# Kernel optimization log

Hardware: AMD Instinct MI355X
Metric: run time of the kernel (lower is better)

## Reference

```python
import jax, jax.numpy as jnp
import numpy as np
import math

H = 16
D_MODEL = 1024
B, S = 2, 2048

def setup_inputs() -> dict:
    key = jax.random.key(0)
    ks = jax.random.split(key, 7)
    q = jax.random.normal(ks[0], (B, S, D_MODEL), dtype=jnp.float32)
    k = jax.random.normal(ks[1], (B, S, D_MODEL), dtype=jnp.float32)
    v = jax.random.normal(ks[2], (B, S, D_MODEL), dtype=jnp.float32)
    mask = jnp.ones((1, 1, S, S), dtype=jnp.int32)
    sc = 1.0 / math.sqrt(D_MODEL)
    W_Q = jax.random.normal(ks[3], (D_MODEL, D_MODEL), dtype=jnp.float32) * sc
    W_K = jax.random.normal(ks[4], (D_MODEL, D_MODEL), dtype=jnp.float32) * sc
    W_V = jax.random.normal(ks[5], (D_MODEL, D_MODEL), dtype=jnp.float32) * sc
    W_T = jax.random.normal(ks[6], (D_MODEL, D_MODEL), dtype=jnp.float32) * sc
    return {"q": q, "k": k, "v": v, "mask": mask, "W_Q": W_Q, "W_K": W_K, "W_V": W_V, "W_T": W_T}

def reference(q, k, v, mask, W_Q, W_K, W_V, W_T):
    # W matrices stored as (in, out); nn.Linear applies x @ W.T with W (out,in),
    # equivalent here since we treat these directly as projection matrices.
    def split_heads(x):  # [B,S,D] -> [B,H,S,hd]
        Bq, Sq, Dq = x.shape
        return x.reshape(Bq, Sq, H, Dq // H).transpose(0, 2, 1, 3)

    Q = split_heads(q @ W_Q)
    K = split_heads(k @ W_K)
    V = split_heads(v @ W_V)
    d_k = Q.shape[-1]
    score = jnp.einsum("bhqd,bhkd->bhqk", Q, K) / math.sqrt(d_k)
    score = jnp.where(mask == 0, jnp.float32(-1e9), score)
    attn = jax.nn.softmax(score, axis=-1)
    out = jnp.einsum("bhqk,bhkd->bhqd", attn, V)
    out = out.transpose(0, 2, 1, 3).reshape(q.shape[0], q.shape[1], D_MODEL)
    return out @ W_T
```

## Files before the change

kernel.cpp:

```cpp
#include <hip/hip_runtime.h>
#include <hip/hip_bf16.h>
#include <stdint.h>

#define H  16
#define DM 1024
#define BB 2
#define SS 2048
#define HD 64

#define QSCALE 0.18033688011112042f
#define MASKVAL -57.7078f

typedef __attribute__((ext_vector_type(8))) short bf16x8;
typedef __attribute__((ext_vector_type(4))) float f32x4;

__device__ __forceinline__ short f2bf(float f) {
  __hip_bfloat16 h = __float2bfloat16(f);
  return *reinterpret_cast<short*>(&h);
}

__device__ __forceinline__ unsigned pack_bf16(float a, float b) {
#if __has_builtin(__builtin_amdgcn_cvt_pk_bf16_f32)
  typedef __attribute__((ext_vector_type(2))) __bf16 bf16x2_t;
  bf16x2_t p = __builtin_amdgcn_cvt_pk_bf16_f32(a, b);
  unsigned u;
  __builtin_memcpy(&u, &p, 4);
  return u;
#else
  unsigned ua = __builtin_bit_cast(unsigned, a);
  unsigned ub = __builtin_bit_cast(unsigned, b);
  ua = (ua + 0x7FFFu + ((ua >> 16) & 1u)) >> 16;
  ub = (ub + 0x7FFFu + ((ub >> 16) & 1u));
  return (ub & 0xFFFF0000u) | ua;
#endif
}

__device__ __forceinline__ void load16_lds(const short* g, short* l) {
  __builtin_amdgcn_global_load_lds(
      (const __attribute__((address_space(1))) void*)g,
      (__attribute__((address_space(3))) void*)l, 16, 0, 0);
}

__global__ void prep_kernel(const float* __restrict__ Wq, const float* __restrict__ Wk,
                            const float* __restrict__ Wv, const float* __restrict__ Wt,
                            short* __restrict__ WTall,
                            const float* __restrict__ q, const float* __restrict__ k,
                            const float* __restrict__ v, short* __restrict__ Abf,
                            const int4* __restrict__ mask4, int* __restrict__ flag) {
  int z = blockIdx.z;
  int t = threadIdx.x;
  if (z < 4) {
    if (blockIdx.x >= 1024) return;
    __shared__ short tile[32][33];
    const float* src = (z == 0) ? Wq : (z == 1) ? Wk : (z == 2) ? Wv : Wt;
    short* out = WTall + (size_t)z * DM * DM;
    int c0 = (blockIdx.x & 31) * 32, r0 = (blockIdx.x >> 5) * 32;
    int tx = t & 31, ty = t >> 5;
    for (int j = 0; j < 4; j++)
      tile[ty + j * 8][tx] = f2bf(src[(size_t)(r0 + ty + j * 8) * DM + c0 + tx]);
    __syncthreads();
    for (int j = 0; j < 4; j++)
      out[(size_t)(c0 + ty + j * 8) * DM + r0 + tx] = tile[tx][ty + j * 8];
  } else if (z < 7) {
    int zz = z - 4;
    const float* src = (zz == 0) ? q : (zz == 1) ? k : v;
    short* out = Abf + (size_t)zz * BB * SS * DM;
    size_t i = ((size_t)blockIdx.x * 256 + t) * 4;
    float4 f = *(const float4*)&src[i];
    uint2 p = {pack_bf16(f.x, f.y), pack_bf16(f.z, f.w)};
    *(uint2*)&out[i] = p;
  } else {
    int idx = blockIdx.x * 256 + t;
    int4 m = mask4[idx];
    if (m.x == 0 || m.y == 0 || m.z == 0 || m.w == 0) atomicOr(flag, 1);
  }
}

__global__ void transpose_w_kernel(const float* __restrict__ Wq, const float* __restrict__ Wk,
                                   const float* __restrict__ Wv, const float* __restrict__ Wt,
                                   short* __restrict__ dst, int* __restrict__ flag) {
  if (blockIdx.x == 0 && blockIdx.y == 0 && blockIdx.z == 0 &&
      threadIdx.y == 0 && threadIdx.x < 2) flag[threadIdx.x] = 0;
  __shared__ short tile[32][33];
  int z = blockIdx.z;
  const float* src = (z == 0) ? Wq : (z == 1) ? Wk : (z == 2) ? Wv : Wt;
  short* out = dst + (size_t)z * DM * DM;
  int c0 = blockIdx.x * 32, r0 = blockIdx.y * 32;
  int tx = threadIdx.x, ty = threadIdx.y;
  for (int j = 0; j < 4; j++)
    tile[ty + j * 8][tx] = f2bf(src[(size_t)(r0 + ty + j * 8) * DM + c0 + tx]);
  __syncthreads();
  for (int j = 0; j < 4; j++)
    out[(size_t)(c0 + ty + j * 8) * DM + r0 + tx] = tile[tx][ty + j * 8];
}

__global__ void mask_scan_kernel(const int4* __restrict__ mask4, int n4, int* __restrict__ flag) {
  int idx = blockIdx.x * blockDim.x + threadIdx.x;
  int stride = gridDim.x * blockDim.x;
  int any = 0;
  for (int i = idx; i < n4; i += stride) {
    int4 m = mask4[i];
    if (m.x == 0 || m.y == 0 || m.z == 0 || m.w == 0) any = 1;
  }
  if (any) atomicOr(flag, 1);
}

__global__ void flag_init_kernel(int* flag) { if (threadIdx.x < 2) flag[threadIdx.x] = 0; }

__global__ void signal_fill_kernel(float* __restrict__ out, int n) {
  int i = blockIdx.x * blockDim.x + threadIdx.x;
  if (i < n) out[i] = 1.0f;
}

template <int AF32>
__device__ __forceinline__ void gemm_fast_body(const void* __restrict__ Av,
                                               const short* __restrict__ Bt,
                                               void* __restrict__ Cv, int mode, float scale,
                                               int m0, int n0) {
  __shared__ __align__(16) short As[128 * 64];
  __shared__ __align__(16) short Bs[128 * 64];
  int t = threadIdx.x;
  int lane = t & 63, w = t >> 6;
  int l16 = lane & 15, quad = lane >> 4;
  int wm = (w >> 1) * 64, wn = (w & 1) * 64;
  f32x4 acc[4][4] = {};

  for (int k0 = 0; k0 < DM; k0 += 64) {
    if (AF32) {
      const float* A = (const float*)Av;
#pragma unroll
      for (int i = 0; i < 8; i++) {
        int c = t + i * 256;
        int row = c >> 4, hseg = c & 15;
        int lseg = (hseg >> 1) ^ (row & 7);
        float4 f = *(const float4*)&A[(size_t)(m0 + row) * DM + k0 + hseg * 4];
        uint2 p = {pack_bf16(f.x, f.y), pack_bf16(f.z, f.w)};
        *(uint2*)&As[row * 64 + lseg * 8 + (hseg & 1) * 4] = p;
      }
    } else {
      const short* A = (const short*)Av;
#pragma unroll
      for (int i = 0; i < 4; i++) {
        int c = t + i * 256;
        int row = c >> 3, seg = c & 7;
        int lseg = seg ^ (row & 7);
        load16_lds(&A[(size_t)(m0 + row) * DM + k0 + lseg * 8], &As[c * 8]);
      }
    }
#pragma unroll
    for (int i = 0; i < 4; i++) {
      int c = t + i * 256;
      int row = c >> 3, seg = c & 7;
      int lseg = seg ^ (row & 7);
      load16_lds(&Bt[(size_t)(n0 + row) * DM + k0 + lseg * 8], &Bs[c * 8]);
    }
    __syncthreads();
#pragma unroll
    for (int h = 0; h < 2; h++) {
      bf16x8 af[4], bfr[4];
#pragma unroll
      for (int i = 0; i < 4; i++)
        af[i] = *(const bf16x8*)&As[(wm + i * 16 + l16) * 64 + (((h * 4 + quad) ^ (l16 & 7)) * 8)];
#pragma unroll
      for (int i = 0; i < 4; i++)
        bfr[i] = *(const bf16x8*)&Bs[(wn + i * 16 + l16) * 64 + (((h * 4 + quad) ^ (l16 & 7)) * 8)];
#pragma unroll
      for (int mi = 0; mi < 4; mi++)
#pragma unroll
        for (int ni = 0; ni < 4; ni++)
          acc[mi][ni] = __builtin_amdgcn_mfma_f32_16x16x32_bf16(af[mi], bfr[ni], acc[mi][ni], 0, 0, 0);
    }
    __syncthreads();
  }

  for (int mi = 0; mi < 4; mi++)
    for (int ni = 0; ni < 4; ni++)
      for (int r = 0; r < 4; r++) {
        int m = m0 + wm + mi * 16 + quad * 4 + r;
        int n = n0 + wn + ni * 16 + l16;
        if (mode == 0) {
          short* C = (short*)Cv;
          int b = m >> 11, s = m & (SS - 1);
          int h = n >> 6, d = n & (HD - 1);
          C[(((size_t)(b * H + h) * SS) + s) * HD + d] = f2bf(acc[mi][ni][r] * scale);
        } else if (mode == 3) {
          short* C = (short*)Cv;
          int h = m >> 6, d = m & (HD - 1);
          int b = n >> 11, s = n & (SS - 1);
          C[((size_t)(b * H + h) * HD + d) * SS + s] = f2bf(acc[mi][ni][r] * scale);
        } else {
          float* C = (float*)Cv;
          C[(size_t)m * DM + n] = acc[mi][ni][r];
        }
      }
}

template <int AF32, int VT>
__global__ __launch_bounds__(256, 2) void gemm_qkv_fast_kernel(
    const void* __restrict__ A0, const void* __restrict__ A1, const void* __restrict__ A2,
    const short* __restrict__ WTall,
    short* __restrict__ Qb, short* __restrict__ Kb, short* __restrict__ Vb) {
  int z = blockIdx.z;
  if (VT && z == 2) {
    gemm_fast_body<0>((const void*)(WTall + 2ull * DM * DM), (const short*)A2, (void*)Vb,
                      3, 1.0f, blockIdx.y * 128, blockIdx.x * 128);
  } else {
    const void* A = (z == 0) ? A0 : (z == 1) ? A1 : A2;
    const short* B = WTall + (size_t)z * DM * DM;
    short* C = (z == 0) ? Qb : (z == 1) ? Kb : Vb;
    gemm_fast_body<AF32>(A, B, (void*)C, 0, (z == 0) ? QSCALE : 1.0f,
                         blockIdx.x * 128, blockIdx.y * 128);
  }
}

__global__ __launch_bounds__(256, 2) void gemm_out_fast_kernel(
    const short* __restrict__ Obuf, const short* __restrict__ WtT, float* __restrict__ out) {
  gemm_fast_body<0>((const void*)Obuf, WtT, (void*)out, 2, 1.0f,
                    blockIdx.x * 128, blockIdx.y * 128);
}

#define LDT 40
#define LDB 136

template <int AF32>
__device__ __forceinline__ void gemm_legacy_body(const void* __restrict__ Av,
                                                 const float* __restrict__ Bm,
                                                 void* __restrict__ Cv, int mode, float scale) {
  __shared__ __align__(16) short As[128 * LDT];
  __shared__ __align__(16) short Bsh[32 * LDB];
  int m0 = blockIdx.x * 128, n0 = blockIdx.y * 128;
  int t = threadIdx.x;
  int lane = t & 63, w = t >> 6;
  int l16 = lane & 15, quad = lane >> 4;
  int wm = (w >> 1) * 64, wn = (w & 1) * 64;
  f32x4 acc[4][4] = {};

  for (int k0 = 0; k0 < DM; k0 += 32) {
    if (AF32) {
      const float* A = (const float*)Av;
      for (int i = 0; i < 4; i++) {
        int c = t + i * 256;
        int row = c >> 3, seg = c & 7;
        float4 f = *(const float4*)&A[(size_t)(m0 + row) * DM + k0 + seg * 4];
        uint2 p = {pack_bf16(f.x, f.y), pack_bf16(f.z, f.w)};
        *(uint2*)&As[row * LDT + seg * 4] = p;
      }
    } else {
      const short* A = (const short*)Av;
      for (int i = 0; i < 2; i++) {
        int c = t + i * 256;
        int row = c >> 2, seg = c & 3;
        *(int4*)&As[row * LDT + seg * 8] = *(const int4*)&A[(size_t)(m0 + row) * DM + k0 + seg * 8];
      }
    }
    for (int i = 0; i < 4; i++) {
      int c = t + i * 256;
      int krow = c >> 5, nseg = c & 31;
      float4 f = *(const float4*)&Bm[(size_t)(k0 + krow) * DM + n0 + nseg * 4];
      uint2 p = {pack_bf16(f.x, f.y), pack_bf16(f.z, f.w)};
      *(uint2*)&Bsh[krow * LDB + nseg * 4] = p;
    }
    __syncthreads();
    bf16x8 af[4], bfr[4];
    for (int i = 0; i < 4; i++) af[i] = *(const bf16x8*)&As[(wm + i * 16 + l16) * LDT + quad * 8];
    for (int i = 0; i < 4; i++) {
      bf16x8 tmp;
      for (int j = 0; j < 8; j++) tmp[j] = Bsh[(quad * 8 + j) * LDB + wn + i * 16 + l16];
      bfr[i] = tmp;
    }
    for (int mi = 0; mi < 4; mi++)
      for (int ni = 0; ni < 4; ni++)
        acc[mi][ni] = __builtin_amdgcn_mfma_f32_16x16x32_bf16(af[mi], bfr[ni], acc[mi][ni], 0, 0, 0);
    __syncthreads();
  }

  for (int mi = 0; mi < 4; mi++)
    for (int ni = 0; ni < 4; ni++)
      for (int r = 0; r < 4; r++) {
        int m = m0 + wm + mi * 16 + quad * 4 + r;
        int n = n0 + wn + ni * 16 + l16;
        if (mode == 0) {
          short* C = (short*)Cv;
          int b = m >> 11, s = m & (SS - 1);
          int h = n >> 6, d = n & (HD - 1);
          C[(((size_t)(b * H + h) * SS) + s) * HD + d] = f2bf(acc[mi][ni][r] * scale);
        } else {
          float* C = (float*)Cv;
          C[(size_t)m * DM + n] = acc[mi][ni][r];
        }
      }
}

__global__ __launch_bounds__(256, 2) void gemm_qkv_legacy_kernel(
    const float* __restrict__ q, const float* __restrict__ k, const float* __restrict__ v,
    const float* __restrict__ B0, const float* __restrict__ B1, const float* __restrict__ B2,
    short* __restrict__ Qb, short* __restrict__ Kb, short* __restrict__ Vb) {
  int z = blockIdx.z;
  const float* A = (z == 0) ? q : (z == 1) ? k : v;
  const float* B = (z == 0) ? B0 : (z == 1) ? B1 : B2;
  short* C = (z == 0) ? Qb : (z == 1) ? Kb : Vb;
  gemm_legacy_body<1>((const void*)A, B, (void*)C, 0, (z == 0) ? QSCALE : 1.0f);
}

__global__ __launch_bounds__(256, 2) void gemm_out_legacy_kernel(
    const short* __restrict__ Obuf, const float* __restrict__ Wt, float* __restrict__ out) {
  gemm_legacy_body<0>((const void*)Obuf, Wt, (void*)out, 2, 1.0f);
}

#define LDP 72

template <int UM>
__device__ __forceinline__ void attn_tile(
    const short* __restrict__ Ksb, const short* __restrict__ Vsb,
    short* __restrict__ Psw, const bf16x8 aq[2], f32x4 oacc[4], float& lsum,
    const int* __restrict__ mask, int qg, int kb) {
  int lane = threadIdx.x & 63;
  int l16 = lane & 15, quad = lane >> 4;

#pragma unroll
  for (int kb2 = 0; kb2 < 4; kb2++) {
    int krow = kb2 * 16 + l16;
    bf16x8 k0 = *(const bf16x8*)&Ksb[krow * 64 + ((quad ^ (l16 & 7)) * 8)];
    bf16x8 k1 = *(const bf16x8*)&Ksb[krow * 64 + (((quad + 4) ^ (l16 & 7)) * 8)];
    f32x4 sc = {};
    sc = __builtin_amdgcn_mfma_f32_16x16x32_bf16(k0, aq[0], sc, 0, 0, 0);
    sc = __builtin_amdgcn_mfma_f32_16x16x32_bf16(k1, aq[1], sc, 0, 0, 0);
    if (UM) {
#pragma unroll
      for (int r = 0; r < 4; r++) {
        int kg = kb + kb2 * 16 + quad * 4 + r;
        if (mask[(size_t)qg * SS + kg] == 0) sc[r] = MASKVAL;
      }
    }
    float p0 = __builtin_exp2f(sc[0]);
    float p1 = __builtin_exp2f(sc[1]);
    float p2 = __builtin_exp2f(sc[2]);
    float p3 = __builtin_exp2f(sc[3]);
    lsum += (p0 + p1) + (p2 + p3);
    uint2 packed = {pack_bf16(p0, p1), pack_bf16(p2, p3)};
    *(uint2*)&Psw[l16 * LDP + kb2 * 16 + quad * 4] = packed;
  }

  __builtin_amdgcn_s_setprio(1);
#pragma unroll
  for (int c = 0; c < 2; c++) {
    bf16x8 ap = *(const bf16x8*)&Psw[l16 * LDP + c * 32 + quad * 8];
#pragma unroll
    for (int nb2 = 0; nb2 < 4; nb2++) {
      bf16x8 bv = *(const bf16x8*)&Vsb[(nb2 * 16 + l16) * 64 + (((c * 4 + quad) ^ (l16 & 7)) * 8)];
      oacc[nb2] = __builtin_amdgcn_mfma_f32_16x16x32_bf16(ap, bv, oacc[nb2], 0, 0, 0);
    }
  }
  __builtin_amdgcn_s_setprio(0);
}

__global__ __launch_bounds__(512, 4) void attn128_kernel(
    const short* __restrict__ Q, const short* __restrict__ K,
    const short* __restrict__ Vt, const int* __restrict__ mask,
    const int* __restrict__ flag, short* __restrict__ O) {
  __shared__ __align__(16) short Ks[2][64 * 64];
  __shared__ __align__(16) short Vs[2][64 * 64];
  __shared__ __align__(16) short Ps[8][16 * LDP];

  int bx = blockIdx.x, by = blockIdx.y;
  int bh = (bx & 7) * 4 + (by >> 3);
  int qt = (by & 7) * 2 + (bx >> 3);
  int q0 = qt * 128;

  int t = threadIdx.x, lane = t & 63, w = t >> 6;
  int l16 = lane & 15, quad = lane >> 4;
  int use_mask = flag[0];

  const short* qrow = Q + ((size_t)bh * SS + q0 + w * 16 + l16) * HD;
  bf16x8 aq[2] = {*(const bf16x8*)&qrow[quad * 8], *(const bf16x8*)&qrow[32 + quad * 8]};

  float lsum = 0.f;
  f32x4 oacc[4] = {};

  const short* Kbase = K  + (size_t)bh * SS * HD;
  const short* Vbase = Vt + (size_t)bh * HD * SS;

  int rp = t >> 3, lc = (t & 7) ^ (rp & 7);
  const short* kSrc = &Kbase[(size_t)rp * HD + lc * 8];
  const short* vSrc = &Vbase[(size_t)rp * SS + lc * 8];
  int qg = q0 + w * 16 + l16;

  load16_lds(kSrc, &Ks[0][t * 8]);
  load16_lds(vSrc, &Vs[0][t * 8]);
  asm volatile("s_waitcnt vmcnt(0)" ::: "memory");
  __builtin_amdgcn_s_barrier();

  int cur = 0;
  if (!use_mask) {
    for (int kt = 0; kt < SS / 64 - 1; kt++) {
      int kb1 = (kt + 1) * 64;
      load16_lds(kSrc + (size_t)kb1 * HD, &Ks[cur ^ 1][t * 8]);
      load16_lds(vSrc + kb1, &Vs[cur ^ 1][t * 8]);
      attn_tile<0>(Ks[cur], Vs[cur], Ps[w], aq, oacc, lsum, mask, qg, kt * 64);
      asm volatile("s_waitcnt vmcnt(0)" ::: "memory");
      __builtin_amdgcn_s_barrier();
      cur ^= 1;
    }
    attn_tile<0>(Ks[cur], Vs[cur], Ps[w], aq, oacc, lsum, mask, qg, SS - 64);
  } else {
    for (int kt = 0; kt < SS / 64 - 1; kt++) {
      int kb1 = (kt + 1) * 64;
      load16_lds(kSrc + (size_t)kb1 * HD, &Ks[cur ^ 1][t * 8]);
      load16_lds(vSrc + kb1, &Vs[cur ^ 1][t * 8]);
      attn_tile<1>(Ks[cur], Vs[cur], Ps[w], aq, oacc, lsum, mask, qg, kt * 64);
      asm volatile("s_waitcnt vmcnt(0)" ::: "memory");
      __builtin_amdgcn_s_barrier();
      cur ^= 1;
    }
    attn_tile<1>(Ks[cur], Vs[cur], Ps[w], aq, oacc, lsum, mask, qg, SS - 64);
  }

  lsum += __shfl_xor(lsum, 16);
  lsum += __shfl_xor(lsum, 32);

  int b = bh >> 4, h = bh & 15;
#pragma unroll
  for (int r = 0; r < 4; r++) {
    float inv = 1.0f / __shfl(lsum, quad * 4 + r);
    int qq = q0 + w * 16 + quad * 4 + r;
#pragma unroll
    for (int nb2 = 0; nb2 < 4; nb2++) {
      int d = nb2 * 16 + l16;
      O[((size_t)(b * SS + qq)) * DM + h * HD + d] = f2bf(oacc[nb2][r] * inv);
    }
  }
}

__global__ __launch_bounds__(256, 4) void attn64_kernel(
    const short* __restrict__ Q, const short* __restrict__ K,
    const short* __restrict__ V, const int* __restrict__ mask,
    const int* __restrict__ flag, short* __restrict__ O) {
  __shared__ __align__(16) short Ks[64 * 64];
  __shared__ __align__(16) short Vs[64 * 64];
  __shared__ __align__(16) short Ps[4][16 * LDP];

  int bh = blockIdx.y;
  int q0 = blockIdx.x * 64;
  int t = threadIdx.x, lane = t & 63, w = t >> 6;
  int l16 = lane & 15, quad = lane >> 4;
  int use_mask = flag[0];

  const short* qrow = Q + ((size_t)bh * SS + q0 + w * 16 + l16) * HD;
  bf16x8 aq0 = *(const bf16x8*)&qrow[quad * 8];
  bf16x8 aq1 = *(const bf16x8*)&qrow[32 + quad * 8];

  float lsum[4] = {0.f, 0.f, 0.f, 0.f};
  f32x4 oacc[4] = {};

  const short* Kbase = K + (size_t)bh * SS * HD;
  const short* Vbase = V + (size_t)bh * SS * HD;
  int dd = t & 63, h2 = t >> 6;

  for (int kt = 0; kt < SS / 64; kt++) {
    int kb = kt * 64;
    for (int i = 0; i < 2; i++) {
      int p = t + i * 256;
      int rp = p >> 3, cp = p & 7;
      int lc = cp ^ (rp & 7);
      load16_lds(&Kbase[(size_t)(kb + rp) * HD + lc * 8], &Ks[p * 8]);
    }
    for (int sgi = 0; sgi < 2; sgi++) {
      int sg = h2 * 2 + sgi;
      short tmp[8];
      for (int jj = 0; jj < 8; jj++)
        tmp[jj] = Vbase[(size_t)(kb + sg * 8 + jj) * HD + dd];
      *(int4*)&Vs[dd * 64 + ((sg ^ (dd & 7)) * 8)] = *(const int4*)tmp;
    }
    __syncthreads();

    for (int nb = 0; nb < 4; nb++) {
      f32x4 sc = {};
      bf16x8 bk0 = *(const bf16x8*)&Ks[(nb * 16 + l16) * 64 + ((quad ^ (l16 & 7)) * 8)];
      bf16x8 bk1 = *(const bf16x8*)&Ks[(nb * 16 + l16) * 64 + (((quad + 4) ^ (l16 & 7)) * 8)];
      sc = __builtin_amdgcn_mfma_f32_16x16x32_bf16(aq0, bk0, sc, 0, 0, 0);
      sc = __builtin_amdgcn_mfma_f32_16x16x32_bf16(aq1, bk1, sc, 0, 0, 0);
      if (use_mask) {
        int kg = kb + nb * 16 + l16;
        for (int r = 0; r < 4; r++) {
          int qg = q0 + w * 16 + quad * 4 + r;
          if (mask[(size_t)qg * SS + kg] == 0) sc[r] = MASKVAL;
        }
      }
      for (int r = 0; r < 4; r++) {
        float pv = __builtin_exp2f(sc[r]);
        lsum[r] += pv;
        Ps[w][(quad * 4 + r) * LDP + nb * 16 + l16] = f2bf(pv);
      }
    }

    for (int c = 0; c < 2; c++) {
      bf16x8 ap = *(const bf16x8*)&Ps[w][l16 * LDP + c * 32 + quad * 8];
      for (int nb2 = 0; nb2 < 4; nb2++) {
        bf16x8 bv = *(const bf16x8*)&Vs[(nb2 * 16 + l16) * 64 + (((c * 4 + quad) ^ (l16 & 7)) * 8)];
        oacc[nb2] = __builtin_amdgcn_mfma_f32_16x16x32_bf16(ap, bv, oacc[nb2], 0, 0, 0);
      }
    }
    __syncthreads();
  }

  for (int st = 1; st < 16; st <<= 1)
    for (int r = 0; r < 4; r++) lsum[r] += __shfl_xor(lsum[r], st);

  int b = bh >> 4, h = bh & 15;
  for (int r = 0; r < 4; r++) {
    float inv = 1.0f / lsum[r];
    int qg = q0 + w * 16 + quad * 4 + r;
    for (int nb2 = 0; nb2 < 4; nb2++) {
      int d = nb2 * 16 + l16;
      O[((size_t)(b * SS + qg)) * DM + h * HD + d] = f2bf(oacc[nb2][r] * inv);
    }
  }
}

extern "C" void kernel_launch(void* const* d_in, const int* in_sizes, int n_in,
                              void* d_out, int out_size, void* d_ws, size_t ws_size,
                              hipStream_t stream) {
  const float* q    = (const float*)d_in[0];
  const float* k    = (const float*)d_in[1];
  const float* v    = (const float*)d_in[2];
  const int*   mask = (const int*)d_in[3];
  const float* Wq   = (const float*)d_in[4];
  const float* Wk   = (const float*)d_in[5];
  const float* Wv   = (const float*)d_in[6];
  const float* Wt   = (const float*)d_in[7];
  float* out = (float*)d_out;

  char* ws = (char*)d_ws;
  const size_t MB = 1024ull * 1024ull;
  const size_t NEED_A = 66 * MB;
  const size_t NEED_B = 40 * MB + 4096;
  const size_t NEED_C = 32 * MB + 4096;

  if (ws_size >= NEED_A) {
    short* WTall = (short*)(ws);
    short* Qbuf  = (short*)(ws + 8 * MB);
    short* Kbuf  = (short*)(ws + 16 * MB);
    short* Vtbuf = (short*)(ws + 24 * MB);
    short* Obuf  = (short*)(ws + 32 * MB);
    int*   flag  = (int*)(ws + 40 * MB);
    short* Abf   = (short*)(ws + 41 * MB);

    hipMemsetAsync(flag, 0, 8, stream);
    prep_kernel<<<dim3(4096, 1, 8), 256, 0, stream>>>(
        Wq, Wk, Wv, Wt, WTall, q, k, v, Abf, (const int4*)mask, flag);
    gemm_qkv_fast_kernel<0, 1><<<dim3(BB * SS / 128, DM / 128, 3), 256, 0, stream>>>(
        Abf, Abf + (size_t)BB * SS * DM, Abf + 2ull * BB * SS * DM, WTall, Qbuf, Kbuf, Vtbuf);
    attn128_kernel<<<dim3(SS / 128, BB * H), 512, 0, stream>>>(Qbuf, Kbuf, Vtbuf, mask, flag, Obuf);
    gemm_out_fast_kernel<<<dim3(BB * SS / 128, DM / 128), 256, 0, stream>>>(
        Obuf, WTall + 3ull * DM * DM, out);
  } else if (ws_size >= NEED_B) {
    short* WTall = (short*)(ws);
    short* Qbuf  = (short*)(ws + 8 * MB);
    short* Kbuf  = (short*)(ws + 16 * MB);
    short* Vbuf  = (short*)(ws + 24 * MB);
    short* Obuf  = (short*)(ws + 32 * MB);
    int*   flag  = (int*)(ws + 40 * MB);

    transpose_w_kernel<<<dim3(32, 32, 4), dim3(32, 8), 0, stream>>>(Wq, Wk, Wv, Wt, WTall, flag);
    mask_scan_kernel<<<512, 256, 0, stream>>>((const int4*)mask, SS * SS / 4, flag);
    gemm_qkv_fast_kernel<1, 0><<<dim3(BB * SS / 128, DM / 128, 3), 256, 0, stream>>>(
        q, k, v, WTall, Qbuf, Kbuf, Vbuf);
    attn64_kernel<<<dim3(SS / 64, BB * H), 256, 0, stream>>>(Qbuf, Kbuf, Vbuf, mask, flag, Obuf);
    gemm_out_fast_kernel<<<dim3(BB * SS / 128, DM / 128), 256, 0, stream>>>(
        Obuf, WTall + 3ull * DM * DM, out);
  } else if (ws_size >= NEED_C) {
    short* Qbuf = (short*)(ws);
    short* Kbuf = (short*)(ws + 8 * MB);
    short* Vbuf = (short*)(ws + 16 * MB);
    short* Obuf = (short*)(ws + 24 * MB);
    int*   flag = (int*)(ws + 32 * MB);

    flag_init_kernel<<<1, 64, 0, stream>>>(flag);
    mask_scan_kernel<<<512, 256, 0, stream>>>((const int4*)mask, SS * SS / 4, flag);
    gemm_qkv_legacy_kernel<<<dim3(BB * SS / 128, DM / 128, 3), 256, 0, stream>>>(
        q, k, v, Wq, Wk, Wv, Qbuf, Kbuf, Vbuf);
    attn64_kernel<<<dim3(SS / 64, BB * H), 256, 0, stream>>>(Qbuf, Kbuf, Vbuf, mask, flag, Obuf);
    gemm_out_legacy_kernel<<<dim3(BB * SS / 128, DM / 128), 256, 0, stream>>>(Obuf, Wt, out);
  } else {
    signal_fill_kernel<<<(BB * SS * DM + 255) / 256, 256, 0, stream>>>(out, BB * SS * DM);
  }
}
```

Measured before the change: 237.0 us.

## Double-buffer LDS tiles in projection GEMM to overlap loads with MFMA

The projection GEMM body now uses two LDS buffers for the A and B tiles. It issues global-to-LDS loads for the next k-slice before running the MFMAs on the current slice, and replaces the two __syncthreads per iteration with one explicit waitcnt plus barrier. The aim is to hide global load latency behind matrix compute. This doubles LDS use to 64 KB per block, which may reduce occupancy, and it depends on the hand-placed waitcnt being correct for the async LDS loads.

New measurement: 258.6 us. +9.1%, slower.

```diff
diff --git a/kernel.cpp b/kernel.cpp
--- a/kernel.cpp
+++ b/kernel.cpp
@@ -117,15 +117,15 @@
                                                const short* __restrict__ Bt,
                                                void* __restrict__ Cv, int mode, float scale,
                                                int m0, int n0) {
-  __shared__ __align__(16) short As[128 * 64];
-  __shared__ __align__(16) short Bs[128 * 64];
+  __shared__ __align__(16) short As[2][128 * 64];
+  __shared__ __align__(16) short Bs[2][128 * 64];
   int t = threadIdx.x;
   int lane = t & 63, w = t >> 6;
   int l16 = lane & 15, quad = lane >> 4;
   int wm = (w >> 1) * 64, wn = (w & 1) * 64;
   f32x4 acc[4][4] = {};
 
-  for (int k0 = 0; k0 < DM; k0 += 64) {
+  auto stage = [&](int buf, int k0) {
     if (AF32) {
       const float* A = (const float*)Av;
 #pragma unroll
@@ -135,7 +135,7 @@
         int lseg = (hseg >> 1) ^ (row & 7);
         float4 f = *(const float4*)&A[(size_t)(m0 + row) * DM + k0 + hseg * 4];
         uint2 p = {pack_bf16(f.x, f.y), pack_bf16(f.z, f.w)};
-        *(uint2*)&As[row * 64 + lseg * 8 + (hseg & 1) * 4] = p;
+        *(uint2*)&As[buf][row * 64 + lseg * 8 + (hseg & 1) * 4] = p;
       }
     } else {
       const short* A = (const short*)Av;
@@ -144,7 +144,7 @@
         int c = t + i * 256;
         int row = c >> 3, seg = c & 7;
         int lseg = seg ^ (row & 7);
-        load16_lds(&A[(size_t)(m0 + row) * DM + k0 + lseg * 8], &As[c * 8]);
+        load16_lds(&A[(size_t)(m0 + row) * DM + k0 + lseg * 8], &As[buf][c * 8]);
       }
     }
 #pragma unroll
@@ -152,26 +152,43 @@
       int c = t + i * 256;
       int row = c >> 3, seg = c & 7;
       int lseg = seg ^ (row & 7);
-      load16_lds(&Bt[(size_t)(n0 + row) * DM + k0 + lseg * 8], &Bs[c * 8]);
-    }
-    __syncthreads();
+      load16_lds(&Bt[(size_t)(n0 + row) * DM + k0 + lseg * 8], &Bs[buf][c * 8]);
+    }
+  };
+
+  auto compute = [&](int buf) {
 #pragma unroll
     for (int h = 0; h < 2; h++) {
       bf16x8 af[4], bfr[4];
 #pragma unroll
       for (int i = 0; i < 4; i++)
-        af[i] = *(const bf16x8*)&As[(wm + i * 16 + l16) * 64 + (((h * 4 + quad) ^ (l16 & 7)) * 8)];
+        af[i] = *(const bf16x8*)&As[buf][(wm + i * 16 + l16) * 64 + (((h * 4 + quad) ^ (l16 & 7)) * 8)];
 #pragma unroll
       for (int i = 0; i < 4; i++)
-        bfr[i] = *(const bf16x8*)&Bs[(wn + i * 16 + l16) * 64 + (((h * 4 + quad) ^ (l16 & 7)) * 8)];
+        bfr[i] = *(const bf16x8*)&Bs[buf][(wn + i * 16 + l16) * 64 + (((h * 4 + quad) ^ (l16 & 7)) * 8)];
 #pragma unroll
       for (int mi = 0; mi < 4; mi++)
 #pragma unroll
         for (int ni = 0; ni < 4; ni++)
           acc[mi][ni] = __builtin_amdgcn_mfma_f32_16x16x32_bf16(af[mi], bfr[ni], acc[mi][ni], 0, 0, 0);
     }
-    __syncthreads();
-  }
+  };
+
+  stage(0, 0);
+  asm volatile("s_waitcnt vmcnt(0)" ::: "memory");
+  if (AF32) asm volatile("s_waitcnt lgkmcnt(0)" ::: "memory");
+  __builtin_amdgcn_s_barrier();
+
+  int cur = 0;
+  for (int k0 = 64; k0 < DM; k0 += 64) {
+    stage(cur ^ 1, k0);
+    compute(cur);
+    asm volatile("s_waitcnt vmcnt(0)" ::: "memory");
+    if (AF32) asm volatile("s_waitcnt lgkmcnt(0)" ::: "memory");
+    __builtin_amdgcn_s_barrier();
+    cur ^= 1;
+  }
+  compute(cur);
 
   for (int mi = 0; mi < 4; mi++)
     for (int ni = 0; ni < 4; ni++)
```
